# Optimization experiments

Hardware: AMD Instinct MI355X
Metric: run time of the kernel (lower is better)

## Reference

```python
import jax, jax.numpy as jnp
import numpy as np

RATIO = 0.5  # init arg of CAGPool_layer
B, N_PER_GRAPH, D, DEG = 256, 512, 256, 32


def setup_inputs() -> dict:
    key = jax.random.key(0)
    k1, k2, k3, k4 = jax.random.split(key, 4)
    N = B * N_PER_GRAPH
    Eg = N_PER_GRAPH * DEG  # edges per graph
    x = jax.random.normal(k1, (N, D), dtype=jnp.float32)
    # within-graph random edges, then offset to global node ids
    src = jax.random.randint(k2, (B, Eg), 0, N_PER_GRAPH, dtype=jnp.int32)
    dst = jax.random.randint(k3, (B, Eg), 0, N_PER_GRAPH, dtype=jnp.int32)
    off = (jnp.arange(B, dtype=jnp.int32) * N_PER_GRAPH)[:, None]
    edge_index = jnp.stack([(src + off).reshape(-1), (dst + off).reshape(-1)], axis=0)
    batch = jnp.repeat(jnp.arange(B, dtype=jnp.int32), N_PER_GRAPH)
    pool_vector = jax.random.normal(k4, (B, D), dtype=jnp.float32)
    c_size = jnp.full((B,), N_PER_GRAPH, dtype=jnp.int32)  # uniform graph sizes
    return {"x": x, "edge_index": edge_index, "batch": batch,
            "pool_vector": pool_vector, "c_size": c_size}


def reference(x, edge_index, batch, pool_vector, c_size):
    N, d = x.shape
    Bn = pool_vector.shape[0]
    n = N // Bn  # uniform nodes per graph (c_size is constant = n)
    k = int(np.ceil(RATIO * n))

    # x_ = pool_vector repeated c_size[i] times == gather by batch (uniform sizes)
    x_ = pool_vector[batch]                                   # [N, d]
    score = jnp.sum(x * x_, axis=1) / jnp.linalg.norm(x_, axis=1)  # [N]

    # per-graph top-k (dense [B, n] view; graphs are contiguous blocks of n nodes)
    _, idx = jax.lax.top_k(score.reshape(Bn, n), k)           # [B, k] local ids
    perm = (idx + (jnp.arange(Bn, dtype=idx.dtype) * n)[:, None]).reshape(-1)  # [B*k]

    # gather kept nodes, sigmoid-gate by their scores
    x_out = x[perm] * jax.nn.sigmoid(score[perm])[:, None]    # [B*k, d]
    batch_out = batch[perm]                                   # [B*k]

    # filter_adj: remap node ids, mask edges with a dropped endpoint.
    # (torch version compacts the edge list; we keep static shape [2, E] and
    #  mark dropped edges with -1 plus a boolean validity mask.)
    nodemap = jnp.full((N,), -1, dtype=jnp.int32).at[perm].set(
        jnp.arange(perm.shape[0], dtype=jnp.int32))
    row = nodemap[edge_index[0]]
    col = nodemap[edge_index[1]]
    valid = (row >= 0) & (col >= 0)
    edge_index_new = jnp.stack([jnp.where(valid, row, -1),
                                jnp.where(valid, col, -1)], axis=0)
    return x_out, edge_index_new, batch_out, perm, valid
```

## Files before the change

### kernel.cpp

```cpp
#include <hip/hip_runtime.h>
#include <math.h>


__global__ __launch_bounds__(1024)
void mega_kernel(const float4* __restrict__ x4,
                 const float4* __restrict__ pool4,
                 const int4* __restrict__ ei_src4,
                 const int4* __restrict__ ei_dst4,
                 float4* __restrict__ out0,
                 float4* __restrict__ out_row,
                 float4* __restrict__ out_col,
                 float4* __restrict__ out_valid,
                 float* __restrict__ out_batch,
                 float* __restrict__ out_perm,
                 int n, int k, int Eg4) {
    __shared__ double s[1024];
    __shared__ int    nmap[1024];
    __shared__ int    perm_l[512];
    __shared__ float  gate_l[512];

    const int b = blockIdx.x;
    const int t = threadIdx.x;
    const int w = t >> 6, l = t & 63;
    const int nw = blockDim.x >> 6;

    float4 pv = pool4[(size_t)b * 64 + l];
    double px = pv.x, py = pv.y, pz = pv.z, pw = pv.w;
    double nn = px * px + py * py + pz * pz + pw * pw;
    for (int off = 32; off > 0; off >>= 1) nn += __shfl_xor(nn, off, 64);
    double inv = 1.0 / sqrt(nn);

    const int npw = n / nw;
    const float4* xg = x4 + ((size_t)b * n + (size_t)w * npw) * 64;

    float4 va = xg[l], vb = xg[64 + l], vc = xg[128 + l], vd = xg[192 + l];
    for (int i = 0; i < npw; i += 4) {
        float4 na, nb, nc, nd;
        bool more = (i + 4 < npw);
        if (more) {
            const float4* xn = xg + (size_t)(i + 4) * 64;
            na = xn[l]; nb = xn[64 + l]; nc = xn[128 + l]; nd = xn[192 + l];
        }
        double da = (double)va.x * px + (double)va.y * py
                  + (double)va.z * pz + (double)va.w * pw;
        double db = (double)vb.x * px + (double)vb.y * py
                  + (double)vb.z * pz + (double)vb.w * pw;
        double dc = (double)vc.x * px + (double)vc.y * py
                  + (double)vc.z * pz + (double)vc.w * pw;
        double dd = (double)vd.x * px + (double)vd.y * py
                  + (double)vd.z * pz + (double)vd.w * pw;
        for (int off = 32; off > 0; off >>= 1) {
            da += __shfl_xor(da, off, 64);
            db += __shfl_xor(db, off, 64);
            dc += __shfl_xor(dc, off, 64);
            dd += __shfl_xor(dd, off, 64);
        }
        if (l == 0) {
            int base = w * npw + i;
            s[base]     = da * inv;
            s[base + 1] = db * inv;
            s[base + 2] = dc * inv;
            s[base + 3] = dd * inv;
        }
        if (more) { va = na; vb = nb; vc = nc; vd = nd; }
    }
    __syncthreads();

    if (t < n) {
        double st = s[t];
        int rank = 0;
#pragma unroll 8
        for (int j = 0; j < n; ++j) {
            double sj = s[j];
            rank += (int)((sj > st) || (sj == st && j < t));
        }
        if (rank < k) {
            int p = b * k + rank;
            nmap[t] = p;
            perm_l[rank] = t;
            gate_l[rank] = (float)(1.0 / (1.0 + exp(-st)));
            out_batch[p] = (float)b;
            out_perm[p]  = (float)(b * n + t);
        } else {
            nmap[t] = -1;
        }
    }
    __syncthreads();

    {
        const int total = k << 6;
        const size_t xbase = (size_t)b * n * 64;
        const size_t obase = (size_t)b * k * 64;
        for (int c = t; c < total; c += 1024) {
            int row = c >> 6, col = c & 63;
            int gl = perm_l[row];
            float g = gate_l[row];
            float4 v = x4[xbase + (size_t)gl * 64 + col];
            v.x *= g; v.y *= g; v.z *= g; v.w *= g;
            out0[obase + (size_t)row * 64 + col] = v;
        }
    }

    {
        const int base_e4 = b * Eg4;
        const int nbase = b * n;
        for (int i = t; i < Eg4; i += 1024) {
            int4 sv = ei_src4[base_e4 + i];
            int4 dv = ei_dst4[base_e4 + i];
            int r0 = nmap[sv.x - nbase], r1 = nmap[sv.y - nbase];
            int r2 = nmap[sv.z - nbase], r3 = nmap[sv.w - nbase];
            int c0 = nmap[dv.x - nbase], c1 = nmap[dv.y - nbase];
            int c2 = nmap[dv.z - nbase], c3 = nmap[dv.w - nbase];
            bool v0 = (r0 >= 0) & (c0 >= 0);
            bool v1 = (r1 >= 0) & (c1 >= 0);
            bool v2 = (r2 >= 0) & (c2 >= 0);
            bool v3 = (r3 >= 0) & (c3 >= 0);
            float4 rv = { v0 ? (float)r0 : -1.0f, v1 ? (float)r1 : -1.0f,
                          v2 ? (float)r2 : -1.0f, v3 ? (float)r3 : -1.0f };
            float4 cv = { v0 ? (float)c0 : -1.0f, v1 ? (float)c1 : -1.0f,
                          v2 ? (float)c2 : -1.0f, v3 ? (float)c3 : -1.0f };
            float4 vv = { v0 ? 1.0f : 0.0f, v1 ? 1.0f : 0.0f,
                          v2 ? 1.0f : 0.0f, v3 ? 1.0f : 0.0f };
            out_row[base_e4 + i]   = rv;
            out_col[base_e4 + i]   = cv;
            out_valid[base_e4 + i] = vv;
        }
    }
}

__global__ void norm_kernel(const float* __restrict__ pool,
                            double* __restrict__ inv_norm, int D) {
    int b = blockIdx.x;
    int l = threadIdx.x;
    double acc = 0.0;
    for (int j = l; j < D; j += 64) {
        double v = (double)pool[(size_t)b * D + j];
        acc += v * v;
    }
    for (int off = 32; off > 0; off >>= 1) acc += __shfl_down(acc, off, 64);
    if (l == 0) inv_norm[b] = 1.0 / sqrt(acc);
}

__global__ void score_kernel(const float* __restrict__ x,
                             const float* __restrict__ pool,
                             const double* __restrict__ inv_norm,
                             double* __restrict__ scores,
                             int D, int n) {
    int node = blockIdx.x * 4 + (threadIdx.x >> 6);
    int l = threadIdx.x & 63;
    int b = node / n;
    const float* xr = x + (size_t)node * D;
    const float* pr = pool + (size_t)b * D;
    double acc = 0.0;
    for (int j = l; j < D; j += 64)
        acc += (double)xr[j] * (double)pr[j];
    for (int off = 32; off > 0; off >>= 1) acc += __shfl_down(acc, off, 64);
    if (l == 0) scores[node] = acc * inv_norm[b];
}

__global__ void rank_kernel(const double* __restrict__ scores,
                            int* __restrict__ nodemap,
                            int* __restrict__ perm_int,
                            float* __restrict__ out,
                            long off_batch, long off_perm,
                            int n, int k) {
    extern __shared__ double sdyn[];
    int b = blockIdx.x;
    int t = threadIdx.x;
    int gid = b * n + t;
    double st = scores[gid];
    sdyn[t] = st;
    __syncthreads();
    int rank = 0;
    for (int j = 0; j < n; ++j) {
        double sj = sdyn[j];
        rank += (int)((sj > st) || (sj == st && j < t));
    }
    if (rank < k) {
        int p = b * k + rank;
        nodemap[gid] = p;
        perm_int[p] = gid;
        out[off_batch + p] = (float)b;
        out[off_perm + p]  = (float)gid;
    } else {
        nodemap[gid] = -1;
    }
}

__global__ void gather_kernel(const float* __restrict__ x,
                              const double* __restrict__ scores,
                              const int* __restrict__ perm_int,
                              float* __restrict__ out0, int D) {
    int p = blockIdx.x;
    int l = threadIdx.x;
    int gid = perm_int[p];
    double sc = scores[gid];
    float g = (float)(1.0 / (1.0 + exp(-sc)));
    const float* xr = x + (size_t)gid * D;
    float* orow = out0 + (size_t)p * D;
    for (int j = l; j < D; j += 64) orow[j] = xr[j] * g;
}

__global__ void edge_kernel(const int* __restrict__ ei,
                            const int* __restrict__ nodemap,
                            float* __restrict__ out,
                            long off_e, long off_valid, long E) {
    long e = (long)blockIdx.x * blockDim.x + threadIdx.x;
    if (e >= E) return;
    int r = nodemap[ei[e]];
    int c = nodemap[ei[E + e]];
    bool valid = (r >= 0) && (c >= 0);
    out[off_e + e]     = valid ? (float)r : -1.0f;
    out[off_e + E + e] = valid ? (float)c : -1.0f;
    out[off_valid + e] = valid ? 1.0f : 0.0f;
}

extern "C" void kernel_launch(void* const* d_in, const int* in_sizes, int n_in,
                              void* d_out, int out_size, void* d_ws, size_t ws_size,
                              hipStream_t stream) {
    const float* x    = (const float*)d_in[0];
    const int*   ei   = (const int*)d_in[1];
    const float* pool = (const float*)d_in[3];

    const int B = in_sizes[4];
    const int D = in_sizes[3] / B;
    const long N = (long)in_sizes[0] / D;
    const long E = (long)in_sizes[1] / 2;
    const int n = (int)(N / B);
    const int k = (n + 1) / 2;
    const long Eg = E / B;

    float* out = (float*)d_out;
    const long o0 = 0;
    const long o1 = o0 + (long)B * k * D;
    const long o2 = o1 + 2 * E;
    const long o3 = o2 + (long)B * k;
    const long o4 = o3 + (long)B * k;

    bool mega_ok = (D == 256) && (n % 64 == 0) && (n <= 1024) &&
                   (Eg % 4 == 0) && (E % 4 == 0) &&
                   (o1 % 4 == 0) && ((o1 + E) % 4 == 0) && (o4 % 4 == 0);

    if (mega_ok) {
        mega_kernel<<<B, 1024, 0, stream>>>(
            (const float4*)x, (const float4*)pool,
            (const int4*)ei, (const int4*)(ei + E),
            (float4*)(out + o0), (float4*)(out + o1),
            (float4*)(out + o1 + E), (float4*)(out + o4),
            out + o2, out + o3,
            n, k, (int)(Eg / 4));
    } else {
        char* ws = (char*)d_ws;
        double* scores   = (double*)ws;                 ws += (size_t)N * 8;
        double* inv_norm = (double*)ws;                 ws += (size_t)B * 8;
        int*    nodemap  = (int*)ws;                    ws += (size_t)N * 4;
        int*    perm_int = (int*)ws;

        norm_kernel<<<B, 64, 0, stream>>>(pool, inv_norm, D);
        score_kernel<<<(int)(N / 4), 256, 0, stream>>>(
            x, pool, inv_norm, scores, D, n);
        rank_kernel<<<B, n, (size_t)n * sizeof(double), stream>>>(
            scores, nodemap, perm_int, out, o2, o3, n, k);
        gather_kernel<<<(int)((long)B * k), 64, 0, stream>>>(
            x, scores, perm_int, out + o0, D);
        edge_kernel<<<(int)((E + 255) / 256), 256, 0, stream>>>(
            ei, nodemap, out, o1, o4, E);
    }
}
```

Measured before the change: 88.17 us.

## Split edge remapping out of fused kernel into a wide grid-parallel kernel

The single 256-block mega kernel is split in two. The first kernel does scoring, ranking and the gated gather, and now writes the node map to a global workspace. A second kernel with many 256-thread blocks stages each graph's node map in shared memory and remaps its edges. This spreads the large edge stream across far more blocks than the 256 in the old per-graph kernel, and the gather and edge paths now use nontemporal loads and stores and a per-wave unrolled row gather. The cost is an extra launch and a global round trip for the node map, and the fast path now needs k divisible by 64 and edge counts divisible by 2048.

```diff
diff --git a/kernel.cpp b/kernel.cpp
--- a/kernel.cpp
+++ b/kernel.cpp
@@ -2,20 +2,28 @@
 #include <math.h>
 
 
+typedef float  nfloat4 __attribute__((ext_vector_type(4)));
+typedef int    nint4   __attribute__((ext_vector_type(4)));
+
+__device__ __forceinline__ void nt_store4(float4* p, float4 v) {
+    nfloat4 nv = { v.x, v.y, v.z, v.w };
+    __builtin_nontemporal_store(nv, reinterpret_cast<nfloat4*>(p));
+}
+__device__ __forceinline__ int4 nt_load4(const int4* p) {
+    nint4 nv = __builtin_nontemporal_load(reinterpret_cast<const nint4*>(p));
+    int4 r; r.x = nv.x; r.y = nv.y; r.z = nv.z; r.w = nv.w;
+    return r;
+}
+
 __global__ __launch_bounds__(1024)
-void mega_kernel(const float4* __restrict__ x4,
-                 const float4* __restrict__ pool4,
-                 const int4* __restrict__ ei_src4,
-                 const int4* __restrict__ ei_dst4,
-                 float4* __restrict__ out0,
-                 float4* __restrict__ out_row,
-                 float4* __restrict__ out_col,
-                 float4* __restrict__ out_valid,
-                 float* __restrict__ out_batch,
-                 float* __restrict__ out_perm,
-                 int n, int k, int Eg4) {
+void srg_kernel(const float4* __restrict__ x4,
+                const float4* __restrict__ pool4,
+                int* __restrict__ nodemap,
+                float4* __restrict__ out0,
+                float* __restrict__ out_batch,
+                float* __restrict__ out_perm,
+                int n, int k) {
     __shared__ double s[1024];
-    __shared__ int    nmap[1024];
     __shared__ int    perm_l[512];
     __shared__ float  gate_l[512];
 
@@ -76,56 +84,101 @@
         }
         if (rank < k) {
             int p = b * k + rank;
-            nmap[t] = p;
+            nodemap[b * n + t] = p;
             perm_l[rank] = t;
             gate_l[rank] = (float)(1.0 / (1.0 + exp(-st)));
             out_batch[p] = (float)b;
             out_perm[p]  = (float)(b * n + t);
         } else {
-            nmap[t] = -1;
+            nodemap[b * n + t] = -1;
         }
     }
     __syncthreads();
 
     {
-        const int total = k << 6;
         const size_t xbase = (size_t)b * n * 64;
         const size_t obase = (size_t)b * k * 64;
-        for (int c = t; c < total; c += 1024) {
-            int row = c >> 6, col = c & 63;
-            int gl = perm_l[row];
-            float g = gate_l[row];
-            float4 v = x4[xbase + (size_t)gl * 64 + col];
-            v.x *= g; v.y *= g; v.z *= g; v.w *= g;
-            out0[obase + (size_t)row * 64 + col] = v;
-        }
-    }
-
-    {
-        const int base_e4 = b * Eg4;
-        const int nbase = b * n;
-        for (int i = t; i < Eg4; i += 1024) {
-            int4 sv = ei_src4[base_e4 + i];
-            int4 dv = ei_dst4[base_e4 + i];
-            int r0 = nmap[sv.x - nbase], r1 = nmap[sv.y - nbase];
-            int r2 = nmap[sv.z - nbase], r3 = nmap[sv.w - nbase];
-            int c0 = nmap[dv.x - nbase], c1 = nmap[dv.y - nbase];
-            int c2 = nmap[dv.z - nbase], c3 = nmap[dv.w - nbase];
-            bool v0 = (r0 >= 0) & (c0 >= 0);
-            bool v1 = (r1 >= 0) & (c1 >= 0);
-            bool v2 = (r2 >= 0) & (c2 >= 0);
-            bool v3 = (r3 >= 0) & (c3 >= 0);
-            float4 rv = { v0 ? (float)r0 : -1.0f, v1 ? (float)r1 : -1.0f,
-                          v2 ? (float)r2 : -1.0f, v3 ? (float)r3 : -1.0f };
-            float4 cv = { v0 ? (float)c0 : -1.0f, v1 ? (float)c1 : -1.0f,
-                          v2 ? (float)c2 : -1.0f, v3 ? (float)c3 : -1.0f };
-            float4 vv = { v0 ? 1.0f : 0.0f, v1 ? 1.0f : 0.0f,
-                          v2 ? 1.0f : 0.0f, v3 ? 1.0f : 0.0f };
-            out_row[base_e4 + i]   = rv;
-            out_col[base_e4 + i]   = cv;
-            out_valid[base_e4 + i] = vv;
-        }
-    }
+        const int rpw = k / 16;
+        const int rbase = w * rpw;
+        for (int i = 0; i < rpw; i += 4) {
+            int r0 = rbase + i;
+            int g0 = perm_l[r0],     g1 = perm_l[r0 + 1];
+            int g2 = perm_l[r0 + 2], g3 = perm_l[r0 + 3];
+            float f0 = gate_l[r0],     f1 = gate_l[r0 + 1];
+            float f2 = gate_l[r0 + 2], f3 = gate_l[r0 + 3];
+            float4 v0 = x4[xbase + (size_t)g0 * 64 + l];
+            float4 v1 = x4[xbase + (size_t)g1 * 64 + l];
+            float4 v2 = x4[xbase + (size_t)g2 * 64 + l];
+            float4 v3 = x4[xbase + (size_t)g3 * 64 + l];
+            v0.x *= f0; v0.y *= f0; v0.z *= f0; v0.w *= f0;
+            v1.x *= f1; v1.y *= f1; v1.z *= f1; v1.w *= f1;
+            v2.x *= f2; v2.y *= f2; v2.z *= f2; v2.w *= f2;
+            v3.x *= f3; v3.y *= f3; v3.z *= f3; v3.w *= f3;
+            nt_store4(&out0[obase + (size_t)(r0    ) * 64 + l], v0);
+            nt_store4(&out0[obase + (size_t)(r0 + 1) * 64 + l], v1);
+            nt_store4(&out0[obase + (size_t)(r0 + 2) * 64 + l], v2);
+            nt_store4(&out0[obase + (size_t)(r0 + 3) * 64 + l], v3);
+        }
+    }
+}
+
+__global__ __launch_bounds__(256)
+void edge_out_kernel(const int4* __restrict__ ei_src,
+                     const int4* __restrict__ ei_dst,
+                     const int* __restrict__ nodemap,
+                     float4* __restrict__ out_row,
+                     float4* __restrict__ out_col,
+                     float4* __restrict__ out_valid,
+                     long epg4, int n) {
+    __shared__ int smem[1024];
+    long e4base = (long)blockIdx.x * 512;
+    long g = e4base / epg4;
+    int base = (int)(g * (long)n);
+    long e0 = e4base + threadIdx.x;
+    long e1 = e0 + 256;
+    int4 s0 = nt_load4(&ei_src[e0]);
+    int4 s1 = nt_load4(&ei_src[e1]);
+    int4 d0 = nt_load4(&ei_dst[e0]);
+    int4 d1 = nt_load4(&ei_dst[e1]);
+    for (int i = threadIdx.x; i < n; i += 256)
+        smem[i] = nodemap[base + i];
+    __syncthreads();
+
+    int r0 = smem[s0.x - base], r1 = smem[s0.y - base];
+    int r2 = smem[s0.z - base], r3 = smem[s0.w - base];
+    int c0 = smem[d0.x - base], c1 = smem[d0.y - base];
+    int c2 = smem[d0.z - base], c3 = smem[d0.w - base];
+    bool v0 = (r0 >= 0) & (c0 >= 0);
+    bool v1 = (r1 >= 0) & (c1 >= 0);
+    bool v2 = (r2 >= 0) & (c2 >= 0);
+    bool v3 = (r3 >= 0) & (c3 >= 0);
+    float4 rv = { v0 ? (float)r0 : -1.0f, v1 ? (float)r1 : -1.0f,
+                  v2 ? (float)r2 : -1.0f, v3 ? (float)r3 : -1.0f };
+    float4 cv = { v0 ? (float)c0 : -1.0f, v1 ? (float)c1 : -1.0f,
+                  v2 ? (float)c2 : -1.0f, v3 ? (float)c3 : -1.0f };
+    float4 vv = { v0 ? 1.0f : 0.0f, v1 ? 1.0f : 0.0f,
+                  v2 ? 1.0f : 0.0f, v3 ? 1.0f : 0.0f };
+    nt_store4(&out_row[e0], rv);
+    nt_store4(&out_col[e0], cv);
+    nt_store4(&out_valid[e0], vv);
+
+    int q0 = smem[s1.x - base], q1 = smem[s1.y - base];
+    int q2 = smem[s1.z - base], q3 = smem[s1.w - base];
+    int u0 = smem[d1.x - base], u1 = smem[d1.y - base];
+    int u2 = smem[d1.z - base], u3 = smem[d1.w - base];
+    bool w0 = (q0 >= 0) & (u0 >= 0);
+    bool w1 = (q1 >= 0) & (u1 >= 0);
+    bool w2 = (q2 >= 0) & (u2 >= 0);
+    bool w3 = (q3 >= 0) & (u3 >= 0);
+    float4 rv1 = { w0 ? (float)q0 : -1.0f, w1 ? (float)q1 : -1.0f,
+                   w2 ? (float)q2 : -1.0f, w3 ? (float)q3 : -1.0f };
+    float4 cv1 = { w0 ? (float)u0 : -1.0f, w1 ? (float)u1 : -1.0f,
+                   w2 ? (float)u2 : -1.0f, w3 ? (float)u3 : -1.0f };
+    float4 vv1 = { w0 ? 1.0f : 0.0f, w1 ? 1.0f : 0.0f,
+                   w2 ? 1.0f : 0.0f, w3 ? 1.0f : 0.0f };
+    nt_store4(&out_row[e1], rv1);
+    nt_store4(&out_col[e1], cv1);
+    nt_store4(&out_valid[e1], vv1);
 }
 
 __global__ void norm_kernel(const float* __restrict__ pool,
@@ -230,6 +283,12 @@
     const int k = (n + 1) / 2;
     const long Eg = E / B;
 
+    char* ws = (char*)d_ws;
+    double* scores   = (double*)ws;                 ws += (size_t)N * 8;
+    double* inv_norm = (double*)ws;                 ws += (size_t)B * 8;
+    int*    nodemap  = (int*)ws;                    ws += (size_t)N * 4;
+    int*    perm_int = (int*)ws;
+
     float* out = (float*)d_out;
     const long o0 = 0;
     const long o1 = o0 + (long)B * k * D;
@@ -237,25 +296,19 @@
     const long o3 = o2 + (long)B * k;
     const long o4 = o3 + (long)B * k;
 
-    bool mega_ok = (D == 256) && (n % 64 == 0) && (n <= 1024) &&
-                   (Eg % 4 == 0) && (E % 4 == 0) &&
+    bool fast_ok = (D == 256) && (n % 64 == 0) && (n <= 1024) && (k % 64 == 0) &&
+                   (E % 2048 == 0) && (Eg % 2048 == 0) &&
                    (o1 % 4 == 0) && ((o1 + E) % 4 == 0) && (o4 % 4 == 0);
 
-    if (mega_ok) {
-        mega_kernel<<<B, 1024, 0, stream>>>(
-            (const float4*)x, (const float4*)pool,
-            (const int4*)ei, (const int4*)(ei + E),
-            (float4*)(out + o0), (float4*)(out + o1),
-            (float4*)(out + o1 + E), (float4*)(out + o4),
-            out + o2, out + o3,
-            n, k, (int)(Eg / 4));
+    if (fast_ok) {
+        srg_kernel<<<B, 1024, 0, stream>>>(
+            (const float4*)x, (const float4*)pool, nodemap,
+            (float4*)(out + o0), out + o2, out + o3, n, k);
+        edge_out_kernel<<<(int)(E / 2048), 256, 0, stream>>>(
+            (const int4*)ei, (const int4*)(ei + E), nodemap,
+            (float4*)(out + o1), (float4*)(out + o1 + E), (float4*)(out + o4),
+            Eg / 4, n);
     } else {
-        char* ws = (char*)d_ws;
-        double* scores   = (double*)ws;                 ws += (size_t)N * 8;
-        double* inv_norm = (double*)ws;                 ws += (size_t)B * 8;
-        int*    nodemap  = (int*)ws;                    ws += (size_t)N * 4;
-        int*    perm_int = (int*)ws;
-
         norm_kernel<<<B, 64, 0, stream>>>(pool, inv_norm, D);
         score_kernel<<<(int)(N / 4), 256, 0, stream>>>(
             x, pool, inv_norm, scores, D, n);
```

Result: faster. 79.01 us (-10.4%).
